# Performance work log

Hardware: AMD Instinct MI355X
Metric: run time of the kernel (lower is better)

## Reference

```python
import jax, jax.numpy as jnp
import numpy as np

B, S, D, H = 2, 2048, 1024, 16
HD = D // H
BAND_LOWER, BAND_UPPER = -1, 0  # tf.linalg.band_part args -> causal


def _causal_add_mask(seq_len):
    # 1 - band_part(ones, lower, upper); 1 where attention is DISALLOWED
    i = jnp.arange(seq_len)[:, None]
    j = jnp.arange(seq_len)[None, :]
    keep = jnp.ones((seq_len, seq_len), bool)
    if BAND_LOWER >= 0:
        keep = keep & ((i - j) <= BAND_LOWER)
    if BAND_UPPER >= 0:
        keep = keep & ((j - i) <= BAND_UPPER)
    return 1.0 - keep.astype(jnp.float32)


def setup_inputs() -> dict:
    key = jax.random.key(0)
    ks = jax.random.split(key, 5)
    scale = 1.0 / np.sqrt(D)
    return {
        "x": jax.random.normal(ks[0], (B, S, D), jnp.float32),
        "wq": jax.random.normal(ks[1], (D, D), jnp.float32) * scale,
        "bq": jnp.zeros((D,), jnp.float32),
        "wk": jax.random.normal(ks[2], (D, D), jnp.float32) * scale,
        "bk": jnp.zeros((D,), jnp.float32),
        "wv": jax.random.normal(ks[3], (D, D), jnp.float32) * scale,
        "bv": jnp.zeros((D,), jnp.float32),
        "wo": jax.random.normal(ks[4], (D, D), jnp.float32) * scale,
        "bo": jnp.zeros((D,), jnp.float32),
    }


def _split_heads(t):
    # [B, S, D] -> [B, H, S, HD]
    return t.reshape(B, S, H, HD).transpose(0, 2, 1, 3)


def reference(x, wq, bq, wk, bk, wv, bv, wo, bo):
    q = _split_heads(x @ wq + bq)
    k = _split_heads(x @ wk + bk)
    v = _split_heads(x @ wv + bv)
    mask = _causal_add_mask(S)  # [S, S], 1 where masked
    logits = jnp.einsum("bhqd,bhkd->bhqk", q, k) / jnp.sqrt(
        jnp.asarray(HD, jnp.float32)
    )
    logits = logits + mask * -1e9
    attn = jax.nn.softmax(logits, axis=-1)
    out = jnp.einsum("bhqk,bhkd->bhqd", attn, v)  # [B, H, S, HD]
    out = out.transpose(0, 2, 1, 3).reshape(B, S, D)
    return out @ wo + bo
```

## Files before the change

kernel.cpp:

```cpp
#include <hip/hip_runtime.h>

#define S_  2048
#define D_  1024
#define H_  16
#define HD_ 64
#define M_  4096
#define K_  1024
#define NEL 4194304

typedef short  bf16x8 __attribute__((ext_vector_type(8)));
typedef float  f32x4  __attribute__((ext_vector_type(4)));
typedef float  f32x16 __attribute__((ext_vector_type(16)));
typedef unsigned int   u32;
typedef unsigned int   u32x2 __attribute__((ext_vector_type(2)));
typedef unsigned int   u32x4v __attribute__((ext_vector_type(4)));
typedef unsigned short u16;
typedef unsigned short u16x4 __attribute__((ext_vector_type(4)));

#define MFMA16(c,a,b) (c) = __builtin_amdgcn_mfma_f32_16x16x32_bf16((a),(b),(c),0,0,0)
#define MFMA32(c,a,b) (c) = __builtin_amdgcn_mfma_f32_32x32x16_bf16((a),(b),(c),0,0,0)

#define QSCALE 0.18033688011112042f

__device__ __forceinline__ u16 f2bf(float f) {
    union { float f; unsigned u; } v; v.f = f;
    unsigned u = v.u;
    u += 0x7FFFu + ((u >> 16) & 1u);
    return (u16)(u >> 16);
}

__device__ __forceinline__ u32 cvtpk(float lo, float hi) {
    u32 r;
    asm("v_cvt_pk_bf16_f32 %0, %1, %2" : "=v"(r) : "v"(lo), "v"(hi));
    return r;
}

__device__ __forceinline__ u32x2 plswap2(u32 a, u32 b) {
    return __builtin_amdgcn_permlane32_swap(a, b, false, false);
}

__device__ __forceinline__ void gload16(const void* g, void* l) {
    __builtin_amdgcn_global_load_lds(
        (const __attribute__((address_space(1))) unsigned*)g,
        (__attribute__((address_space(3))) unsigned*)l, 16, 0, 0);
}

__global__ __launch_bounds__(256) void cvt_x(const float* __restrict__ x,
                                             u16* __restrict__ xb) {
    const int i = (blockIdx.x * 256 + threadIdx.x) * 8;
    f32x4 a = *(const f32x4*)&x[i];
    f32x4 b = *(const f32x4*)&x[i + 4];
    u16 t[8];
#pragma unroll
    for (int j = 0; j < 4; ++j) { t[j] = f2bf(a[j]); t[4 + j] = f2bf(b[j]); }
    *(bf16x8*)&xb[i] = *(const bf16x8*)t;
}

__global__ __launch_bounds__(256) void cvt_w(const float* __restrict__ w0,
                                             const float* __restrict__ w1,
                                             const float* __restrict__ w2,
                                             const float* __restrict__ w3,
                                             u16* __restrict__ Wt) {
    __shared__ float T[64][65];
    const float* W = blockIdx.z == 0 ? w0 : blockIdx.z == 1 ? w1
                   : blockIdx.z == 2 ? w2 : w3;
    const int k0 = blockIdx.x * 64, n0 = blockIdx.y * 64;
    const int r  = threadIdx.x >> 2, c0 = (threadIdx.x & 3) * 16;
#pragma unroll
    for (int j = 0; j < 4; ++j)
        *(f32x4*)&T[r][c0 + j * 4] = *(const f32x4*)&W[(size_t)(k0 + r) * D_ + n0 + c0 + j * 4];
    __syncthreads();
    u16 tmp[16];
#pragma unroll
    for (int j = 0; j < 16; ++j) tmp[j] = f2bf(T[c0 + j][r]);
    u16* dst = Wt + ((size_t)blockIdx.z * 1024 + n0 + r) * K_ + k0 + c0;
    *(bf16x8*)dst       = *(const bf16x8*)tmp;
    *(bf16x8*)(dst + 8) = *(const bf16x8*)(tmp + 8);
}

template <int BM, int MODE>
__global__ __launch_bounds__(256) void gemm2(
    const u16* __restrict__ A, const u16* __restrict__ Bt,
    const float* __restrict__ b0, const float* __restrict__ b1,
    const float* __restrict__ b2, void* __restrict__ Out)
{
    __shared__ u16 As[BM * 32];
    __shared__ u16 Bs[128 * 32];
    const int tid = threadIdx.x, lane = tid & 63, wid = tid >> 6;
    const int lr = lane & 15, lg = lane >> 4;
    const int n0 = blockIdx.x * 128, m0 = blockIdx.y * BM;
    const int wm = (wid >> 1) * (BM / 2), wn = (wid & 1) * 64;
    const int lrow = lane >> 2, lch = lane & 3;

    f32x4 acc[BM / 32][4] = {};

    for (int k0 = 0; k0 < K_; k0 += 32) {
        __syncthreads();
#pragma unroll
        for (int t = 0; t < BM / 64; ++t) {
            const int row = wid * (BM / 4) + t * 16 + lrow;
            gload16(A + (size_t)(m0 + row) * K_ + k0 + lch * 8,
                    (u16*)As + row * 32 + lch * 8);
        }
#pragma unroll
        for (int t = 0; t < 2; ++t) {
            const int row = wid * 32 + t * 16 + lrow;
            gload16(Bt + (size_t)(n0 + row) * K_ + k0 + lch * 8,
                    (u16*)Bs + row * 32 + lch * 8);
        }
        __syncthreads();

        bf16x8 af[BM / 32], bf[4];
#pragma unroll
        for (int i = 0; i < BM / 32; ++i)
            af[i] = *(const bf16x8*)&As[(wm + i * 16 + lr) * 32 + lg * 8];
#pragma unroll
        for (int j = 0; j < 4; ++j)
            bf[j] = *(const bf16x8*)&Bs[(wn + j * 16 + lr) * 32 + lg * 8];
#pragma unroll
        for (int i = 0; i < BM / 32; ++i)
#pragma unroll
            for (int j = 0; j < 4; ++j) MFMA16(acc[i][j], af[i], bf[j]);
    }

#pragma unroll
    for (int i = 0; i < BM / 32; ++i) {
#pragma unroll
        for (int j = 0; j < 4; ++j) {
            const int n = n0 + wn + j * 16 + lr;
            const int m = m0 + wm + i * 16 + lg * 4;
            if constexpr (MODE == 0) {
                const int which = n >> 10, nn = n & 1023;
                const float* bp = which == 0 ? b0 : which == 1 ? b1 : b2;
                const float bv = bp[nn];
                u16* qkv = (u16*)Out;
                const int h = nn >> 6, hd = nn & 63;
                const int b = m >> 11, s = m & 2047;
                if (which == 2) {
                    u16x4 pk;
#pragma unroll
                    for (int r4 = 0; r4 < 4; ++r4) pk[r4] = f2bf(acc[i][j][r4] + bv);
                    *(u16x4*)&qkv[(size_t)2 * NEL +
                                  ((size_t)(b * H_ + h) * HD_ + hd) * S_ + s] = pk;
                } else {
                    const float sc = (which == 0) ? QSCALE : 1.0f;
                    const size_t bas = (size_t)which * NEL + (size_t)(b * H_ + h) * S_ * HD_;
#pragma unroll
                    for (int r4 = 0; r4 < 4; ++r4)
                        qkv[bas + (size_t)(s + r4) * HD_ + hd] =
                            f2bf((acc[i][j][r4] + bv) * sc);
                }
            } else {
                const float bv = b0[n];
                float* o = (float*)Out;
#pragma unroll
                for (int r4 = 0; r4 < 4; ++r4)
                    o[(size_t)(m + r4) * D_ + n] = acc[i][j][r4] + bv;
            }
        }
    }
}

__global__ __launch_bounds__(128) void attn10(
    const u16* __restrict__ Q, const u16* __restrict__ K,
    const u16* __restrict__ Vt, u16* __restrict__ CTX)
{
    __shared__ float OB[64][33];
    __shared__ float MB[64], LB[64];

    const int tid  = threadIdx.x;
    const int lane = tid & 63, wv = tid >> 6;
    const int lo = lane & 31, hi = lane >> 5;
    const int idx = blockIdx.x;
    const int bh  = idx & 31;
    const int qb  = 63 - (idx >> 5);
    const int wq0 = qb * 32;
    const size_t base  = (size_t)bh * S_ * HD_;
    const size_t vbase = (size_t)bh * HD_ * S_;

    bool flip;
    {
        u32 pa = hi ? 10u : 20u;
        u32 pb = hi ? 30u : 40u;
        u32x2 pr = plswap2(pa, pb);
        flip = (pr[0] == 10u) || (pr[0] == 30u);
    }

    bf16x8 qf[4];
#pragma unroll
    for (int ks = 0; ks < 4; ++ks)
        qf[ks] = *(const bf16x8*)&Q[base + (size_t)(wq0 + lo) * HD_ + ks * 16 + hi * 8];

    f32x16 acc[2] = {};
    float m_ = -1e30f, l_ = 0.f;
    const int nt = (wq0 >> 6) + 1;

    for (int t = wv; t < nt; t += 2) {
        const int kv0 = t * 64;
        const bool sub1 = (kv0 + 32 <= wq0 + 31);

        f32x16 cT[2];
#pragma unroll
        for (int i = 0; i < 16; ++i) { cT[0][i] = 0.f; cT[1][i] = 0.f; }
        __builtin_amdgcn_s_setprio(1);
#pragma unroll
        for (int ks = 0; ks < 4; ++ks) {
            bf16x8 kf = *(const bf16x8*)&K[base + (size_t)(kv0 + lo) * HD_ + ks * 16 + hi * 8];
            MFMA32(cT[0], kf, qf[ks]);
        }
        if (sub1) {
#pragma unroll
            for (int ks = 0; ks < 4; ++ks) {
                bf16x8 kf = *(const bf16x8*)&K[base + (size_t)(kv0 + 32 + lo) * HD_ + ks * 16 + hi * 8];
                MFMA32(cT[1], kf, qf[ks]);
            }
        }
        __builtin_amdgcn_s_setprio(0);

        bf16x8 vf[2][4];
#pragma unroll
        for (int dt = 0; dt < 2; ++dt)
#pragma unroll
            for (int ks = 0; ks < 4; ++ks)
                if (ks < 2 || sub1)
                    vf[dt][ks] = *(const bf16x8*)&Vt[vbase + (size_t)(dt * 32 + lo) * S_ +
                                                     kv0 + ks * 16 + hi * 8];

        if (kv0 + 63 > wq0) {
            const int qg = wq0 + lo;
#pragma unroll
            for (int tt = 0; tt < 2; ++tt)
#pragma unroll
                for (int r = 0; r < 16; ++r) {
                    const int kvg = kv0 + tt * 32 + (r & 3) + 8 * (r >> 2) + 4 * hi;
                    if (kvg > qg) cT[tt][r] = -1e9f;
                }
        }

        float m8[8];
#pragma unroll
        for (int i = 0; i < 8; ++i)
            m8[i] = fmaxf(fmaxf(cT[0][i], cT[0][i + 8]), fmaxf(cT[1][i], cT[1][i + 8]));
        float mx = fmaxf(fmaxf(fmaxf(m8[0], m8[1]), fmaxf(m8[2], m8[3])),
                         fmaxf(fmaxf(m8[4], m8[5]), fmaxf(m8[6], m8[7])));
        mx = fmaxf(mx, __shfl_xor(mx, 32));

        if (!__all(mx <= m_ + 11.5f)) {
            const float mn = fmaxf(m_, mx);
            const float al = exp2f(m_ - mn);
            m_ = mn; l_ *= al;
            float alr[16];
#pragma unroll
            for (int r = 0; r < 16; ++r)
                alr[r] = __shfl(al, (r & 3) + 8 * (r >> 2) + 4 * hi);
#pragma unroll
            for (int r = 0; r < 16; ++r) { acc[0][r] *= alr[r]; acc[1][r] *= alr[r]; }
        }

#pragma unroll
        for (int i = 0; i < 16; ++i) {
            cT[0][i] = exp2f(cT[0][i] - m_);
            cT[1][i] = exp2f(cT[1][i] - m_);
        }
        float s8[8];
#pragma unroll
        for (int i = 0; i < 8; ++i)
            s8[i] = (cT[0][i] + cT[0][i + 8]) + (cT[1][i] + cT[1][i + 8]);
        float ssum = ((s8[0] + s8[1]) + (s8[2] + s8[3])) +
                     ((s8[4] + s8[5]) + (s8[6] + s8[7]));
        ssum += __shfl_xor(ssum, 32);
        l_ += ssum;

        u32 pk[2][8];
#pragma unroll
        for (int tt = 0; tt < 2; ++tt)
#pragma unroll
            for (int w = 0; w < 8; ++w)
                pk[tt][w] = cvtpk(cT[tt][2 * w], cT[tt][2 * w + 1]);

#pragma unroll
        for (int ks = 0; ks < 4; ++ks) {
            if (ks < 2 || sub1) {
                const int tt = ks >> 1;
                const int o4 = (ks & 1) * 4;
                u32x2 s0 = plswap2(pk[tt][o4 + 0], pk[tt][o4 + 2]);
                u32x2 s1 = plswap2(pk[tt][o4 + 1], pk[tt][o4 + 3]);
                u32x4v v;
                v.x = flip ? s0[1] : s0[0];
                v.y = flip ? s1[1] : s1[0];
                v.z = flip ? s0[0] : s0[1];
                v.w = flip ? s1[0] : s1[1];
                const bf16x8 af = __builtin_bit_cast(bf16x8, v);
                __builtin_amdgcn_s_setprio(1);
                MFMA32(acc[0], af, vf[0][ks]);
                MFMA32(acc[1], af, vf[1][ks]);
                __builtin_amdgcn_s_setprio(0);
            }
        }
    }

    if (wv == 1) {
#pragma unroll
        for (int r = 0; r < 16; ++r) {
            OB[lane][r]      = acc[0][r];
            OB[lane][16 + r] = acc[1][r];
        }
        MB[lane] = m_;
        LB[lane] = l_;
    }
    __syncthreads();
    if (wv != 0) return;

    const float m1 = MB[lane], l1 = LB[lane];
    const float mM = fmaxf(m_, m1);
    const float a0 = exp2f(m_ - mM), a1 = exp2f(m1 - mM);
    l_ = l_ * a0 + l1 * a1;
    float a0r[16], a1r[16];
#pragma unroll
    for (int r = 0; r < 16; ++r) {
        const int rq = (r & 3) + 8 * (r >> 2) + 4 * hi;
        a0r[r] = __shfl(a0, rq);
        a1r[r] = __shfl(a1, rq);
    }
#pragma unroll
    for (int r = 0; r < 16; ++r) {
        acc[0][r] = acc[0][r] * a0r[r] + OB[lane][r]      * a1r[r];
        acc[1][r] = acc[1][r] * a0r[r] + OB[lane][16 + r] * a1r[r];
    }

    const float linv = 1.0f / l_;
    float lrr[16];
#pragma unroll
    for (int r = 0; r < 16; ++r)
        lrr[r] = __shfl(linv, (r & 3) + 8 * (r >> 2) + 4 * hi);
    const int b = bh >> 4, h = bh & 15;
#pragma unroll
    for (int r = 0; r < 16; ++r) {
        const int q = wq0 + (r & 3) + 8 * (r >> 2) + 4 * hi;
        u16* o = &CTX[(size_t)(b * S_ + q) * D_ + h * HD_ + lo];
        o[0]  = f2bf(acc[0][r] * lrr[r]);
        o[32] = f2bf(acc[1][r] * lrr[r]);
    }
}

extern "C" void kernel_launch(void* const* d_in, const int* in_sizes, int n_in,
                              void* d_out, int out_size, void* d_ws, size_t ws_size,
                              hipStream_t stream)
{
    const float* x  = (const float*)d_in[0];
    const float* wq = (const float*)d_in[1];
    const float* bq = (const float*)d_in[2];
    const float* wk = (const float*)d_in[3];
    const float* bk = (const float*)d_in[4];
    const float* wv = (const float*)d_in[5];
    const float* bv = (const float*)d_in[6];
    const float* wo = (const float*)d_in[7];
    const float* bo = (const float*)d_in[8];

    char* ws = (char*)d_ws;
    u16*   xb    = (u16*)ws;
    u16*   WtAll = (u16*)(ws + (size_t)8  * 1024 * 1024);
    u16*   qkv   = (u16*)(ws + (size_t)16 * 1024 * 1024);
    u16*   ctx   = xb;

    cvt_x<<<2048, 256, 0, stream>>>(x, xb);
    cvt_w<<<dim3(16, 16, 4), 256, 0, stream>>>(wq, wk, wv, wo, WtAll);

    gemm2<128, 0><<<dim3(24, 32), 256, 0, stream>>>(xb, WtAll, bq, bk, bv, qkv);

    attn10<<<dim3(2048), 128, 0, stream>>>(qkv, qkv + NEL, qkv + 2 * (size_t)NEL, ctx);

    gemm2<64, 1><<<dim3(8, 64), 256, 0, stream>>>(ctx, WtAll + (size_t)3072 * K_,
                                                  bo, bo, bo, d_out);
}
```

Before: 149.3 us.

## Stage K and V tiles into swizzled per-wave LDS before MFMA reads

Each attention wave now copies its 64-row K tile and its V^T tile into its own XOR-swizzled LDS region with a cooperative, row-contiguous load helper, then waits on all loads. The MFMA operand fragments are read from LDS instead of being gathered straight from global memory by every lane. The aim is better-coalesced global traffic and bank-conflict-free fragment reads. In exchange the kernel now reserves 32 KB of LDS per block, which can reduce resident blocks per CU. The full wait on vmcnt(0) with a single buffer also serialises load latency against compute, since the next tile is not prefetched.

```diff
diff --git a/kernel.cpp b/kernel.cpp
--- a/kernel.cpp
+++ b/kernel.cpp
@@ -161,12 +161,11 @@
     }
 }
 
-__global__ __launch_bounds__(128) void attn10(
+__global__ __launch_bounds__(128) void attn11(
     const u16* __restrict__ Q, const u16* __restrict__ K,
     const u16* __restrict__ Vt, u16* __restrict__ CTX)
 {
-    __shared__ float OB[64][33];
-    __shared__ float MB[64], LB[64];
+    __shared__ __align__(16) char SMEM[32768];
 
     const int tid  = threadIdx.x;
     const int lane = tid & 63, wv = tid >> 6;
@@ -178,6 +177,12 @@
     const size_t base  = (size_t)bh * S_ * HD_;
     const size_t vbase = (size_t)bh * HD_ * S_;
 
+    char* Kw = SMEM + wv * 16384;
+    char* Vw = Kw + 8192;
+    float (*OB)[33] = (float (*)[33])(SMEM + 16384);
+    float* MBp = (float*)(SMEM + 16384 + 8448);
+    float* LBp = MBp + 64;
+
     bool flip;
     {
         u32 pa = hi ? 10u : 20u;
@@ -186,6 +191,10 @@
         flip = (pr[0] == 10u) || (pr[0] == 30u);
     }
 
+    const int r8  = lane >> 3;
+    const int csw = (lane & 7) ^ r8;
+    const int swz = lo & 7;
+
     bf16x8 qf[4];
 #pragma unroll
     for (int ks = 0; ks < 4; ++ks)
@@ -199,19 +208,33 @@
         const int kv0 = t * 64;
         const bool sub1 = (kv0 + 32 <= wq0 + 31);
 
+        {
+            const u16* kSrc = K  + base  + (size_t)(kv0 + r8) * HD_ + csw * 8;
+            const u16* vSrc = Vt + vbase + (size_t)r8 * S_ + kv0 + csw * 8;
+            char* kDst = Kw + (lane << 4);
+            char* vDst = Vw + (lane << 4);
+            const int ni = sub1 ? 8 : 4;
+            for (int i = 0; i < ni; ++i)
+                gload16(kSrc + (size_t)(i * 8) * HD_, kDst + i * 1024);
+#pragma unroll
+            for (int i = 0; i < 8; ++i)
+                gload16(vSrc + (size_t)(i * 8) * S_, vDst + i * 1024);
+            asm volatile("s_waitcnt vmcnt(0)" ::: "memory");
+        }
+
         f32x16 cT[2];
 #pragma unroll
         for (int i = 0; i < 16; ++i) { cT[0][i] = 0.f; cT[1][i] = 0.f; }
         __builtin_amdgcn_s_setprio(1);
 #pragma unroll
         for (int ks = 0; ks < 4; ++ks) {
-            bf16x8 kf = *(const bf16x8*)&K[base + (size_t)(kv0 + lo) * HD_ + ks * 16 + hi * 8];
+            bf16x8 kf = *(const bf16x8*)(Kw + (lo << 7) + (((2 * ks + hi) ^ swz) << 4));
             MFMA32(cT[0], kf, qf[ks]);
         }
         if (sub1) {
 #pragma unroll
             for (int ks = 0; ks < 4; ++ks) {
-                bf16x8 kf = *(const bf16x8*)&K[base + (size_t)(kv0 + 32 + lo) * HD_ + ks * 16 + hi * 8];
+                bf16x8 kf = *(const bf16x8*)(Kw + ((32 + lo) << 7) + (((2 * ks + hi) ^ swz) << 4));
                 MFMA32(cT[1], kf, qf[ks]);
             }
         }
@@ -223,8 +246,8 @@
 #pragma unroll
             for (int ks = 0; ks < 4; ++ks)
                 if (ks < 2 || sub1)
-                    vf[dt][ks] = *(const bf16x8*)&Vt[vbase + (size_t)(dt * 32 + lo) * S_ +
-                                                     kv0 + ks * 16 + hi * 8];
+                    vf[dt][ks] = *(const bf16x8*)(Vw + ((dt * 32 + lo) << 7) +
+                                                  (((2 * ks + hi) ^ swz) << 4));
 
         if (kv0 + 63 > wq0) {
             const int qg = wq0 + lo;
@@ -305,13 +328,13 @@
             OB[lane][r]      = acc[0][r];
             OB[lane][16 + r] = acc[1][r];
         }
-        MB[lane] = m_;
-        LB[lane] = l_;
+        MBp[lane] = m_;
+        LBp[lane] = l_;
     }
     __syncthreads();
     if (wv != 0) return;
 
-    const float m1 = MB[lane], l1 = LB[lane];
+    const float m1 = MBp[lane], l1 = LBp[lane];
     const float mM = fmaxf(m_, m1);
     const float a0 = exp2f(m_ - mM), a1 = exp2f(m1 - mM);
     l_ = l_ * a0 + l1 * a1;
@@ -368,7 +391,7 @@
 
     gemm2<128, 0><<<dim3(24, 32), 256, 0, stream>>>(xb, WtAll, bq, bk, bv, qkv);
 
-    attn10<<<dim3(2048), 128, 0, stream>>>(qkv, qkv + NEL, qkv + 2 * (size_t)NEL, ctx);
+    attn11<<<dim3(2048), 128, 0, stream>>>(qkv, qkv + NEL, qkv + 2 * (size_t)NEL, ctx);
 
     gemm2<64, 1><<<dim3(8, 64), 256, 0, stream>>>(ctx, WtAll + (size_t)3072 * K_,
                                                   bo, bo, bo, d_out);
```

Result: faster. 134.7 us (-9.8%).

## Share K/V tiles across four query waves via double-buffered swizzled LDS

Applied to the files above, without the earlier changes.

The attention kernel moves from two waves splitting the KV range of one 32-row query block to four waves each owning its own 32-row query block within a 128-row group. K and V tiles are staged cooperatively into double-buffered, XOR-swizzled shared memory with async global loads and reused by all four waves, instead of every wave reading K and V directly from global memory. This drops the cross-wave softmax merge at the end. The cost is a block-wide barrier every tile and idle waves on diagonal tiles, plus a grid four times smaller.

```diff
diff --git a/kernel.cpp b/kernel.cpp
--- a/kernel.cpp
+++ b/kernel.cpp
@@ -161,20 +161,19 @@
     }
 }
 
-__global__ __launch_bounds__(128) void attn10(
+__global__ __launch_bounds__(256) void attn15(
     const u16* __restrict__ Q, const u16* __restrict__ K,
     const u16* __restrict__ Vt, u16* __restrict__ CTX)
 {
-    __shared__ float OB[64][33];
-    __shared__ float MB[64], LB[64];
+    __shared__ __align__(16) char SMEM[2][16384];
 
     const int tid  = threadIdx.x;
     const int lane = tid & 63, wv = tid >> 6;
     const int lo = lane & 31, hi = lane >> 5;
     const int idx = blockIdx.x;
     const int bh  = idx & 31;
-    const int qb  = 63 - (idx >> 5);
-    const int wq0 = qb * 32;
+    const int qg  = 15 - (idx >> 5);
+    const int wq0 = qg * 128 + wv * 32;
     const size_t base  = (size_t)bh * S_ * HD_;
     const size_t vbase = (size_t)bh * HD_ * S_;
 
@@ -186,6 +185,28 @@
         flip = (pr[0] == 10u) || (pr[0] == 30u);
     }
 
+    const int srow = tid >> 3;
+    const int sch  = tid & 7;
+    const int swz  = lo & 7;
+
+    auto stage = [&](char* buf, int t) {
+        const int kv0s = t * 64;
+#pragma unroll
+        for (int i = 0; i < 2; ++i) {
+            const int r  = srow + i * 32;
+            const int cs = sch ^ (r & 7);
+            gload16(K + base + (size_t)(kv0s + r) * HD_ + cs * 8,
+                    buf + tid * 16 + i * 4096);
+        }
+#pragma unroll
+        for (int i = 0; i < 2; ++i) {
+            const int r  = srow + i * 32;
+            const int cs = sch ^ (r & 7);
+            gload16(Vt + vbase + (size_t)r * S_ + kv0s + cs * 8,
+                    buf + 8192 + tid * 16 + i * 4096);
+        }
+    };
+
     bf16x8 qf[4];
 #pragma unroll
     for (int ks = 0; ks < 4; ++ks)
@@ -193,139 +214,121 @@
 
     f32x16 acc[2] = {};
     float m_ = -1e30f, l_ = 0.f;
-    const int nt = (wq0 >> 6) + 1;
-
-    for (int t = wv; t < nt; t += 2) {
+    const int ntmax = qg * 2 + 2;
+
+    stage(SMEM[0], 0);
+
+    for (int t = 0; t < ntmax; ++t) {
         const int kv0 = t * 64;
-        const bool sub1 = (kv0 + 32 <= wq0 + 31);
-
-        f32x16 cT[2];
-#pragma unroll
-        for (int i = 0; i < 16; ++i) { cT[0][i] = 0.f; cT[1][i] = 0.f; }
-        __builtin_amdgcn_s_setprio(1);
-#pragma unroll
-        for (int ks = 0; ks < 4; ++ks) {
-            bf16x8 kf = *(const bf16x8*)&K[base + (size_t)(kv0 + lo) * HD_ + ks * 16 + hi * 8];
-            MFMA32(cT[0], kf, qf[ks]);
-        }
-        if (sub1) {
+        char* Kw = SMEM[t & 1];
+        char* Vw = Kw + 8192;
+
+        asm volatile("s_waitcnt vmcnt(0)" ::: "memory");
+        __syncthreads();
+        if (t + 1 < ntmax) stage(SMEM[(t + 1) & 1], t + 1);
+
+        if (kv0 <= wq0 + 31) {
+            const bool sub1 = (kv0 + 32 <= wq0 + 31);
+
+            f32x16 cT[2];
+#pragma unroll
+            for (int i = 0; i < 16; ++i) { cT[0][i] = 0.f; cT[1][i] = 0.f; }
+            __builtin_amdgcn_s_setprio(1);
 #pragma unroll
             for (int ks = 0; ks < 4; ++ks) {
-                bf16x8 kf = *(const bf16x8*)&K[base + (size_t)(kv0 + 32 + lo) * HD_ + ks * 16 + hi * 8];
-                MFMA32(cT[1], kf, qf[ks]);
-            }
-        }
-        __builtin_amdgcn_s_setprio(0);
-
-        bf16x8 vf[2][4];
-#pragma unroll
-        for (int dt = 0; dt < 2; ++dt)
-#pragma unroll
-            for (int ks = 0; ks < 4; ++ks)
-                if (ks < 2 || sub1)
-                    vf[dt][ks] = *(const bf16x8*)&Vt[vbase + (size_t)(dt * 32 + lo) * S_ +
-                                                     kv0 + ks * 16 + hi * 8];
-
-        if (kv0 + 63 > wq0) {
-            const int qg = wq0 + lo;
+                bf16x8 kf = *(const bf16x8*)(Kw + (lo << 7) + (((2 * ks + hi) ^ swz) << 4));
+                MFMA32(cT[0], kf, qf[ks]);
+            }
+            if (sub1) {
+#pragma unroll
+                for (int ks = 0; ks < 4; ++ks) {
+                    bf16x8 kf = *(const bf16x8*)(Kw + ((32 + lo) << 7) + (((2 * ks + hi) ^ swz) << 4));
+                    MFMA32(cT[1], kf, qf[ks]);
+                }
+            }
+            __builtin_amdgcn_s_setprio(0);
+
+            bf16x8 vf[2][4];
+#pragma unroll
+            for (int dt = 0; dt < 2; ++dt)
+#pragma unroll
+                for (int ks = 0; ks < 4; ++ks)
+                    if (ks < 2 || sub1)
+                        vf[dt][ks] = *(const bf16x8*)(Vw + ((dt * 32 + lo) << 7) +
+                                                      (((2 * ks + hi) ^ swz) << 4));
+
+            if (kv0 + 63 > wq0) {
+                const int qgl = wq0 + lo;
+#pragma unroll
+                for (int tt = 0; tt < 2; ++tt)
+#pragma unroll
+                    for (int r = 0; r < 16; ++r) {
+                        const int kvg = kv0 + tt * 32 + (r & 3) + 8 * (r >> 2) + 4 * hi;
+                        if (kvg > qgl) cT[tt][r] = -1e9f;
+                    }
+            }
+
+            float m8[8];
+#pragma unroll
+            for (int i = 0; i < 8; ++i)
+                m8[i] = fmaxf(fmaxf(cT[0][i], cT[0][i + 8]), fmaxf(cT[1][i], cT[1][i + 8]));
+            float mx = fmaxf(fmaxf(fmaxf(m8[0], m8[1]), fmaxf(m8[2], m8[3])),
+                             fmaxf(fmaxf(m8[4], m8[5]), fmaxf(m8[6], m8[7])));
+            mx = fmaxf(mx, __shfl_xor(mx, 32));
+
+            if (!__all(mx <= m_ + 11.5f)) {
+                const float mn = fmaxf(m_, mx);
+                const float al = exp2f(m_ - mn);
+                m_ = mn; l_ *= al;
+                float alr[16];
+#pragma unroll
+                for (int r = 0; r < 16; ++r)
+                    alr[r] = __shfl(al, (r & 3) + 8 * (r >> 2) + 4 * hi);
+#pragma unroll
+                for (int r = 0; r < 16; ++r) { acc[0][r] *= alr[r]; acc[1][r] *= alr[r]; }
+            }
+
+#pragma unroll
+            for (int i = 0; i < 16; ++i) {
+                cT[0][i] = exp2f(cT[0][i] - m_);
+                cT[1][i] = exp2f(cT[1][i] - m_);
+            }
+            float s8[8];
+#pragma unroll
+            for (int i = 0; i < 8; ++i)
+                s8[i] = (cT[0][i] + cT[0][i + 8]) + (cT[1][i] + cT[1][i + 8]);
+            float ssum = ((s8[0] + s8[1]) + (s8[2] + s8[3])) +
+                         ((s8[4] + s8[5]) + (s8[6] + s8[7]));
+            ssum += __shfl_xor(ssum, 32);
+            l_ += ssum;
+
+            u32 pk[2][8];
 #pragma unroll
             for (int tt = 0; tt < 2; ++tt)
 #pragma unroll
-                for (int r = 0; r < 16; ++r) {
-                    const int kvg = kv0 + tt * 32 + (r & 3) + 8 * (r >> 2) + 4 * hi;
-                    if (kvg > qg) cT[tt][r] = -1e9f;
+                for (int w = 0; w < 8; ++w)
+                    pk[tt][w] = cvtpk(cT[tt][2 * w], cT[tt][2 * w + 1]);
+
+#pragma unroll
+            for (int ks = 0; ks < 4; ++ks) {
+                if (ks < 2 || sub1) {
+                    const int tt = ks >> 1;
+                    const int o4 = (ks & 1) * 4;
+                    u32x2 s0 = plswap2(pk[tt][o4 + 0], pk[tt][o4 + 2]);
+                    u32x2 s1 = plswap2(pk[tt][o4 + 1], pk[tt][o4 + 3]);
+                    u32x4v v;
+                    v.x = flip ? s0[1] : s0[0];
+                    v.y = flip ? s1[1] : s1[0];
+                    v.z = flip ? s0[0] : s0[1];
+                    v.w = flip ? s1[0] : s1[1];
+                    const bf16x8 af = __builtin_bit_cast(bf16x8, v);
+                    __builtin_amdgcn_s_setprio(1);
+                    MFMA32(acc[0], af, vf[0][ks]);
+                    MFMA32(acc[1], af, vf[1][ks]);
+                    __builtin_amdgcn_s_setprio(0);
                 }
-        }
-
-        float m8[8];
-#pragma unroll
-        for (int i = 0; i < 8; ++i)
-            m8[i] = fmaxf(fmaxf(cT[0][i], cT[0][i + 8]), fmaxf(cT[1][i], cT[1][i + 8]));
-        float mx = fmaxf(fmaxf(fmaxf(m8[0], m8[1]), fmaxf(m8[2], m8[3])),
-                         fmaxf(fmaxf(m8[4], m8[5]), fmaxf(m8[6], m8[7])));
-        mx = fmaxf(mx, __shfl_xor(mx, 32));
-
-        if (!__all(mx <= m_ + 11.5f)) {
-            const float mn = fmaxf(m_, mx);
-            const float al = exp2f(m_ - mn);
-            m_ = mn; l_ *= al;
-            float alr[16];
-#pragma unroll
-            for (int r = 0; r < 16; ++r)
-                alr[r] = __shfl(al, (r & 3) + 8 * (r >> 2) + 4 * hi);
-#pragma unroll
-            for (int r = 0; r < 16; ++r) { acc[0][r] *= alr[r]; acc[1][r] *= alr[r]; }
-        }
-
-#pragma unroll
-        for (int i = 0; i < 16; ++i) {
-            cT[0][i] = exp2f(cT[0][i] - m_);
-            cT[1][i] = exp2f(cT[1][i] - m_);
-        }
-        float s8[8];
-#pragma unroll
-        for (int i = 0; i < 8; ++i)
-            s8[i] = (cT[0][i] + cT[0][i + 8]) + (cT[1][i] + cT[1][i + 8]);
-        float ssum = ((s8[0] + s8[1]) + (s8[2] + s8[3])) +
-                     ((s8[4] + s8[5]) + (s8[6] + s8[7]));
-        ssum += __shfl_xor(ssum, 32);
-        l_ += ssum;
-
-        u32 pk[2][8];
-#pragma unroll
-        for (int tt = 0; tt < 2; ++tt)
-#pragma unroll
-            for (int w = 0; w < 8; ++w)
-                pk[tt][w] = cvtpk(cT[tt][2 * w], cT[tt][2 * w + 1]);
-
-#pragma unroll
-        for (int ks = 0; ks < 4; ++ks) {
-            if (ks < 2 || sub1) {
-                const int tt = ks >> 1;
-                const int o4 = (ks & 1) * 4;
-                u32x2 s0 = plswap2(pk[tt][o4 + 0], pk[tt][o4 + 2]);
-                u32x2 s1 = plswap2(pk[tt][o4 + 1], pk[tt][o4 + 3]);
-                u32x4v v;
-                v.x = flip ? s0[1] : s0[0];
-                v.y = flip ? s1[1] : s1[0];
-                v.z = flip ? s0[0] : s0[1];
-                v.w = flip ? s1[0] : s1[1];
-                const bf16x8 af = __builtin_bit_cast(bf16x8, v);
-                __builtin_amdgcn_s_setprio(1);
-                MFMA32(acc[0], af, vf[0][ks]);
-                MFMA32(acc[1], af, vf[1][ks]);
-                __builtin_amdgcn_s_setprio(0);
-            }
-        }
-    }
-
-    if (wv == 1) {
-#pragma unroll
-        for (int r = 0; r < 16; ++r) {
-            OB[lane][r]      = acc[0][r];
-            OB[lane][16 + r] = acc[1][r];
-        }
-        MB[lane] = m_;
-        LB[lane] = l_;
-    }
-    __syncthreads();
-    if (wv != 0) return;
-
-    const float m1 = MB[lane], l1 = LB[lane];
-    const float mM = fmaxf(m_, m1);
-    const float a0 = exp2f(m_ - mM), a1 = exp2f(m1 - mM);
-    l_ = l_ * a0 + l1 * a1;
-    float a0r[16], a1r[16];
-#pragma unroll
-    for (int r = 0; r < 16; ++r) {
-        const int rq = (r & 3) + 8 * (r >> 2) + 4 * hi;
-        a0r[r] = __shfl(a0, rq);
-        a1r[r] = __shfl(a1, rq);
-    }
-#pragma unroll
-    for (int r = 0; r < 16; ++r) {
-        acc[0][r] = acc[0][r] * a0r[r] + OB[lane][r]      * a1r[r];
-        acc[1][r] = acc[1][r] * a0r[r] + OB[lane][16 + r] * a1r[r];
+            }
+        }
     }
 
     const float linv = 1.0f / l_;
@@ -368,7 +371,7 @@
 
     gemm2<128, 0><<<dim3(24, 32), 256, 0, stream>>>(xb, WtAll, bq, bk, bv, qkv);
 
-    attn10<<<dim3(2048), 128, 0, stream>>>(qkv, qkv + NEL, qkv + 2 * (size_t)NEL, ctx);
+    attn15<<<dim3(512), 256, 0, stream>>>(qkv, qkv + NEL, qkv + 2 * (size_t)NEL, ctx);
 
     gemm2<64, 1><<<dim3(8, 64), 256, 0, stream>>>(ctx, WtAll + (size_t)3072 * K_,
                                                   bo, bo, bo, d_out);
```

Result: faster. 140.3 us (-6.0%).
